# Kernel optimization log

Measured on AMD Instinct MI355X. Metric: run time of the kernel, lower is better.

## Reference

```python
import jax, jax.numpy as jnp
import numpy as np

N_NODES = 100_000
N_EDGES = 1_000_000
H = 128
NUM_STATES = 4
UPPER_T, LOWER_T, NUM_ITERS, TEMP_EVAL = 1.0, 0.1, 10000, 0.1


def temp_by_step(step, upper, lower, num_iters, temp_eval):
    # Python-level schedule: eval temp at step == -1, else linear anneal.
    if step == -1:
        return temp_eval
    frac = min(step / num_iters, 1.0)
    return upper + (lower - upper) * frac


def from_binary_states(states):
    # [*, k] bits -> integer id in [0, 2**k)
    weights = 2 ** jnp.arange(states.shape[-1])
    return (states * weights).sum(-1)


def setup_inputs() -> dict:
    key = jax.random.key(0)
    ks = jax.random.split(key, 20)
    N, E, h = N_NODES, N_EDGES, H
    node_states = jax.random.randint(ks[0], (N, NUM_STATES), 0, 2)
    edge_states = jax.random.randint(ks[1], (E, NUM_STATES), 0, 2)
    scalars = jax.random.normal(ks[2], (E, 1), jnp.float32)
    # first N edges are self-loops ordered by node id (required by the module's
    # node_scalars = scalars[src == dst] indexing convention)
    loops = jnp.arange(N)
    src = jax.random.randint(ks[3], (E - N,), 0, N)
    dst = jax.random.randint(ks[4], (E - N,), 0, N)
    dst = jnp.where(dst == src, (dst + 1) % N, dst)  # no accidental self-loops
    edge_index = jnp.stack([jnp.concatenate([loops, src]),
                            jnp.concatenate([loops, dst])])
    batched_reverse_idx = jax.random.randint(ks[5], (E,), 0, E)
    batch_scalars = jax.random.normal(ks[6], (E, 1, 1), jnp.float32)
    s = 0.02
    params = dict(
        node_emb=s * jax.random.normal(ks[7], (2 ** NUM_STATES, h), jnp.float32),
        edge_emb=s * jax.random.normal(ks[8], (2 ** NUM_STATES, h), jnp.float32),
        combine_W=s * jax.random.normal(ks[9], (2 * h, h), jnp.float32),
        combine_b=jnp.zeros((h,), jnp.float32),
        keep_W=s * jax.random.normal(ks[10], (h, 2), jnp.float32),
        keep_b=jnp.zeros((2,), jnp.float32),
        push_W=s * jax.random.normal(ks[11], (h, 2), jnp.float32),
        push_b=jnp.zeros((2,), jnp.float32),
        push_node_W=s * jax.random.normal(ks[12], (h, 2), jnp.float32),
        push_node_b=jnp.zeros((2,), jnp.float32),
        increment_W=s * jax.random.normal(ks[13], (h, 2), jnp.float32),
        increment_b=jnp.zeros((2,), jnp.float32),
    )
    return dict(node_states=node_states, edge_states=edge_states, scalars=scalars,
                edge_index=edge_index, batched_reverse_idx=batched_reverse_idx,
                batch_scalars=batch_scalars, processor_step=0, training_step=0,
                **params)


def reference(node_states, edge_states, scalars, edge_index, batched_reverse_idx,
              batch_scalars, processor_step, training_step,
              node_emb, edge_emb, combine_W, combine_b, keep_W, keep_b,
              push_W, push_b, push_node_W, push_node_b,
              increment_W, increment_b):
    N = node_states.shape[0]
    tau = temp_by_step(int(training_step), UPPER_T, LOWER_T, NUM_ITERS, TEMP_EVAL)
    # use_noise = config.use_noise (False) and training_step != -1 -> False

    node_fts = node_emb[from_binary_states(node_states)]   # [N, h]
    edge_fts = edge_emb[from_binary_states(edge_states)]   # [E, h]
    src, dst = edge_index[0], edge_index[1]
    fts = jnp.concatenate([edge_fts[batched_reverse_idx], node_fts[src]], axis=1)
    fts = fts @ combine_W + combine_b                       # [E, h]

    s = scalars.reshape(-1)                                 # [E]

    def pair_gumbel_first(W, b):
        # grouped (per-edge pair) softmax; take first component (== [::2])
        logits = (fts @ W + b) / tau                        # [E, 2]
        return jax.nn.softmax(logits, axis=-1)[:, 0]

    increment = 1.0 * pair_gumbel_first(increment_W, increment_b)
    keep = s * pair_gumbel_first(keep_W, keep_b)

    # push: first N edges are self-loops, self-loop of node i is edge i
    push_wo = pair_gumbel_first(push_W, push_b)
    push_w = pair_gumbel_first(push_node_W, push_node_b)
    node_scalars = s[:N]                                    # scalars at self-loops
    s_wo = s - node_scalars[dst]
    s_w = s_wo + node_scalars[src]
    acc = (jax.ops.segment_sum(push_wo * s_wo, dst, num_segments=N)
           + jax.ops.segment_sum(push_w * s_w, dst, num_segments=N))  # [N]
    edge_push = jnp.zeros_like(s).at[:N].set(acc)           # nonzero only on self-loops

    new_scalars = (increment + keep + edge_push)[:, None]   # [E, 1]
    target = batch_scalars[:, processor_step]               # [E, 1]
    loss = jnp.mean((target - new_scalars) ** 2)
    return new_scalars, loss
```

## Files before the change

kernel.cpp:

```cpp
#include <hip/hip_runtime.h>
#include <math.h>
#include <stdint.h>

#define N_NODES 100000
#define N_EDGES 1000000
#define N_NONLOOP (N_EDGES - N_NODES)
#define NXCD 8

#define NP    16
#define PSZ   6250
#define PCAP  61440
#define GOWN  16
#define PROW  6272

#define ACC_SCALE   1048576.0f
#define ACC_INV     (1.0f / 1048576.0f)

typedef float  vfloat4 __attribute__((ext_vector_type(4)));
typedef int    vint4   __attribute__((ext_vector_type(4)));
typedef unsigned long long u64;

#define XCC_ID_HWREG (20 | ((4 - 1) << 11))
__device__ __forceinline__ int get_xcc() {
    return __builtin_amdgcn_s_getreg(XCC_ID_HWREG) & (NXCD - 1);
}
__device__ __forceinline__ void l2_atomic_add_u32(uint32_t* p, uint32_t v) {
    asm volatile("global_atomic_add %0, %1, off" :: "v"(p), "v"(v) : "memory");
}
__device__ __forceinline__ void l2_atomic_add_f32(float* p, float v) {
    asm volatile("global_atomic_add_f32 %0, %1, off" :: "v"(p), "v"(v) : "memory");
}

__device__ __forceinline__ float get_invtau(const int* __restrict__ training_step) {
    int step = training_step[0];
    float tau;
    if (step == -1) {
        tau = 0.1f;
    } else {
        float frac = fminf((float)step / 10000.0f, 1.0f);
        tau = 1.0f + (0.1f - 1.0f) * frac;
    }
    return 1.0f / tau;
}

__device__ __forceinline__ float wave_reduce(float v) {
    #pragma unroll
    for (int off = 32; off > 0; off >>= 1) v += __shfl_down(v, off, 64);
    return v;
}

#define TAB_BLOCKS  132
#define NODE_BLOCKS 391
#define EI_BLOCKS   977

__global__ __launch_bounds__(256) void fused_pre(
    const int* __restrict__ node_states,
    const int* __restrict__ edge_states,
    const float* __restrict__ node_emb,
    const float* __restrict__ edge_emb,
    const float* __restrict__ cW, const float* __restrict__ cb,
    const float* __restrict__ kW, const float* __restrict__ kb,
    const float* __restrict__ pW, const float* __restrict__ pb,
    const float* __restrict__ pnW, const float* __restrict__ pnb,
    const float* __restrict__ iW, const float* __restrict__ ib,
    const int* __restrict__ tstep,
    uint32_t* __restrict__ acc,
    uint32_t* __restrict__ cnt,
    uint8_t* __restrict__ ei,
    uint8_t* __restrict__ nib,
    float* __restrict__ tabs,
    float* __restrict__ lossp,
    float* __restrict__ loss_out,
    int ncopies)
{
    const int b = blockIdx.x;

    if (b < TAB_BLOCKS) {
        const int w    = b;
        const int lane = threadIdx.x & 63;
        const int wv   = threadIdx.x >> 6;
        const float invtau = get_invtau(tstep);
        __shared__ float part[4];

        float p = 0.f;
        if (w < 128) {
            const int isB = w >> 6, h = (w >> 4) & 3, i = w & 15;
            const float* emb = isB ? node_emb : edge_emb;
            const float* cWh = cW + isB * 128 * 128;
            float t0 = 0.f, t1 = 0.f;
            const int l0 = wv * 32;
            #pragma unroll 8
            for (int l = l0; l < l0 + 32; ++l) {
                const float el = emb[i * 128 + l];
                t0 += el * cWh[l * 128 + lane];
                t1 += el * cWh[l * 128 + 64 + lane];
            }
            const float* W = (h == 0) ? kW : (h == 1) ? pW : (h == 2) ? pnW : iW;
            const float wd0 = W[2 * lane] - W[2 * lane + 1];
            const float wd1 = W[2 * (lane + 64)] - W[2 * (lane + 64) + 1];
            p = t0 * wd0 + t1 * wd1;
        } else if (wv == 0) {
            const int h = w & 3;
            const float* W = (h == 0) ? kW : (h == 1) ? pW : (h == 2) ? pnW : iW;
            const float wd0 = W[2 * lane] - W[2 * lane + 1];
            const float wd1 = W[2 * (lane + 64)] - W[2 * (lane + 64) + 1];
            p = cb[lane] * wd0 + cb[64 + lane] * wd1;
        }
        p = wave_reduce(p);
        if (lane == 0) part[wv] = p;
        __syncthreads();
        if (threadIdx.x == 0) {
            const float tot = part[0] + part[1] + part[2] + part[3];
            if (w < 128) {
                const int isB = w >> 6, h = (w >> 4) & 3, i = w & 15;
                tabs[isB * 64 + i * 4 + h] = tot * invtau;
            } else {
                const int h = w & 3;
                const float* bb = (h == 0) ? kb : (h == 1) ? pb : (h == 2) ? pnb : ib;
                tabs[128 + h] = (tot + bb[0] - bb[1]) * invtau;
            }
        }
        return;
    }

    if (b < TAB_BLOCKS + NODE_BLOCKS) {
        const int n = (b - TAB_BLOCKS) * 256 + threadIdx.x;
        if (n < 256) lossp[n] = 0.f;
        if (n == 0) *loss_out = 0.f;
        if (ncopies == 0) {
            if (n < NP) cnt[n] = 0u;
        }
        if (n < N_NODES) {
            vint4 st = __builtin_nontemporal_load(&((const vint4*)node_states)[n]);
            nib[n] = (uint8_t)(st.x + 2 * st.y + 4 * st.z + 8 * st.w);
            for (int k = 0; k < ncopies; ++k) acc[(size_t)k * N_NODES + n] = 0u;
        }
        return;
    }

    const int t = (b - TAB_BLOCKS - NODE_BLOCKS) * 256 + threadIdx.x;
    if (t < N_EDGES / 4) {
        const vint4* esp = (const vint4*)edge_states + 4 * t;
        vint4 e0 = __builtin_nontemporal_load(esp + 0);
        vint4 e1 = __builtin_nontemporal_load(esp + 1);
        vint4 e2 = __builtin_nontemporal_load(esp + 2);
        vint4 e3 = __builtin_nontemporal_load(esp + 3);
        const uint32_t i0 = e0.x + 2 * e0.y + 4 * e0.z + 8 * e0.w;
        const uint32_t i1 = e1.x + 2 * e1.y + 4 * e1.z + 8 * e1.w;
        const uint32_t i2 = e2.x + 2 * e2.y + 4 * e2.z + 8 * e2.w;
        const uint32_t i3 = e3.x + 2 * e3.y + 4 * e3.z + 8 * e3.w;
        ((uint32_t*)ei)[t] = i0 | (i1 << 8) | (i2 << 16) | (i3 << 24);
    }
}

#define EPT 8
__global__ __launch_bounds__(256) void edge_compact(
    const float* __restrict__ s,
    const int* __restrict__ src,
    const int* __restrict__ dst,
    const int* __restrict__ brev,
    const uint8_t* __restrict__ ei,
    const uint8_t* __restrict__ nib,
    const float* __restrict__ tabs,
    const float* __restrict__ target,
    uint32_t* __restrict__ cnt,
    u64* __restrict__ pairs,
    float* __restrict__ lossp,
    float* __restrict__ out)
{
    __shared__ float4 sf[33];
    __shared__ uint32_t lbase[NP], loff[NP];
    const int tid = threadIdx.x;
    if (tid < 33) sf[tid] = ((const float4*)tabs)[tid];
    if (tid < NP) loff[tid] = 0u;
    __syncthreads();

    const int t = blockIdx.x * 256 + tid;
    const bool active = (t < N_NONLOOP / EPT);
    float lsum = 0.f;
    float    ov[EPT], av[EPT];
    int      pj[EPT];
    uint32_t kj[EPT], dloc[EPT];
    int g0 = 0;

    if (active) {
        g0 = (N_NODES / 4) + 2 * t;
        const vint4   rva = __builtin_nontemporal_load(&((const vint4*)brev)[g0]);
        const vint4   rvb = __builtin_nontemporal_load(&((const vint4*)brev)[g0 + 1]);
        const vint4   sra = __builtin_nontemporal_load(&((const vint4*)src)[g0]);
        const vint4   srb = __builtin_nontemporal_load(&((const vint4*)src)[g0 + 1]);
        const vint4   dsa = __builtin_nontemporal_load(&((const vint4*)dst)[g0]);
        const vint4   dsb = __builtin_nontemporal_load(&((const vint4*)dst)[g0 + 1]);
        const vfloat4 sva = __builtin_nontemporal_load(&((const vfloat4*)s)[g0]);
        const vfloat4 svb = __builtin_nontemporal_load(&((const vfloat4*)s)[g0 + 1]);
        const vfloat4 tga = __builtin_nontemporal_load(&((const vfloat4*)target)[g0]);
        const vfloat4 tgb = __builtin_nontemporal_load(&((const vfloat4*)target)[g0 + 1]);

        const int rvv[EPT] = {rva.x, rva.y, rva.z, rva.w, rvb.x, rvb.y, rvb.z, rvb.w};
        const int srv[EPT] = {sra.x, sra.y, sra.z, sra.w, srb.x, srb.y, srb.z, srb.w};
        const int dsv[EPT] = {dsa.x, dsa.y, dsa.z, dsa.w, dsb.x, dsb.y, dsb.z, dsb.w};
        const float svv[EPT] = {sva.x, sva.y, sva.z, sva.w, svb.x, svb.y, svb.z, svb.w};
        const float tgv[EPT] = {tga.x, tga.y, tga.z, tga.w, tgb.x, tgb.y, tgb.z, tgb.w};

        int   eidx[EPT], ni[EPT];
        float ss[EPT], sd[EPT];
        #pragma unroll
        for (int j = 0; j < EPT; ++j) {
            eidx[j] = ei[rvv[j]];
            ni[j]   = nib[srv[j]];
            ss[j]   = s[srv[j]];
            sd[j]   = s[dsv[j]];
        }

        const float4 c4 = sf[32];
        #pragma unroll
        for (int j = 0; j < EPT; ++j) {
            const float4 a = sf[eidx[j]];
            const float4 b = sf[16 + ni[j]];
            const float lk  = a.x + b.x + c4.x;
            const float lp  = a.y + b.y + c4.y;
            const float lpn = a.z + b.z + c4.z;
            const float li  = a.w + b.w + c4.w;
            const float pk  = 1.f / (1.f + __expf(-lk));
            const float pp  = 1.f / (1.f + __expf(-lp));
            const float ppn = 1.f / (1.f + __expf(-lpn));
            const float pi  = 1.f / (1.f + __expf(-li));

            const float s_wo = svv[j] - sd[j];
            const float s_w  = s_wo + ss[j];
            av[j] = pp * s_wo + ppn * s_w;

            const uint32_t p = (uint32_t)dsv[j] / (uint32_t)PSZ;
            pj[j]   = (int)p;
            dloc[j] = (uint32_t)dsv[j] - p * (uint32_t)PSZ;

            ov[j] = pi + svv[j] * pk;
            const float d = tgv[j] - ov[j];
            lsum += d * d;
        }

        #pragma unroll
        for (int j = 0; j < EPT; ++j) kj[j] = atomicAdd(&loff[pj[j]], 1u);
    }

    __syncthreads();
    if (tid < NP) lbase[tid] = atomicAdd(&cnt[tid], loff[tid]);
    __syncthreads();

    if (active) {
        #pragma unroll
        for (int j = 0; j < EPT; ++j) {
            const uint32_t slot = lbase[pj[j]] + kj[j];
            if (slot < PCAP)
                pairs[(size_t)pj[j] * PCAP + slot] =
                    ((u64)dloc[j] << 32) | (uint32_t)__float_as_int(av[j]);
        }
        vfloat4 o4a = {ov[0], ov[1], ov[2], ov[3]};
        vfloat4 o4b = {ov[4], ov[5], ov[6], ov[7]};
        __builtin_nontemporal_store(o4a, &((vfloat4*)out)[g0]);
        __builtin_nontemporal_store(o4b, &((vfloat4*)out)[g0 + 1]);
    }

    lsum = wave_reduce(lsum);
    if ((tid & 63) == 0)
        atomicAdd(&lossp[(blockIdx.x & 15) * 16], lsum);
}

__global__ __launch_bounds__(256) void bin_accum(
    const u64* __restrict__ pairs,
    const uint32_t* __restrict__ cnt,
    float* __restrict__ partials)
{
    __shared__ float part[PROW];
    const int tid = threadIdx.x;
    const int p = blockIdx.x >> 4, r = blockIdx.x & 15;

    for (int k = tid; k < PROW; k += 256) part[k] = 0.f;
    __syncthreads();

    uint32_t c = cnt[p];
    if (c > PCAP) c = PCAP;
    const uint32_t chunk = (c + GOWN - 1) / GOWN;
    const uint32_t lo = r * chunk;
    uint32_t hi = lo + chunk;
    if (hi > c) hi = c;

    const u64* pp = pairs + (size_t)p * PCAP;
    for (uint32_t i = lo + tid; i < hi; i += 256) {
        const u64 v = pp[i];
        atomicAdd(&part[(uint32_t)(v >> 32)], __int_as_float((int)(uint32_t)v));
    }
    __syncthreads();

    float* row = partials + (size_t)blockIdx.x * PROW;
    for (int k = tid; k < PSZ; k += 256) row[k] = part[k];
}

__global__ __launch_bounds__(256) void finalize_binned(
    const float* __restrict__ s,
    const int* __restrict__ brev,
    const uint8_t* __restrict__ ei,
    const uint8_t* __restrict__ nib,
    const float* __restrict__ tabs,
    const float* __restrict__ target,
    const float* __restrict__ partials,
    const float* __restrict__ lossp,
    float* __restrict__ out,
    float* __restrict__ loss_out)
{
    __shared__ float4 sf[33];
    if (threadIdx.x < 33) sf[threadIdx.x] = ((const float4*)tabs)[threadIdx.x];
    __syncthreads();

    const int n = blockIdx.x * blockDim.x + threadIdx.x;
    const bool active = (n < N_NODES);
    float sq = 0.f, v = 0.f;
    if (active) {
        const int  eidx = ei[brev[n]];
        const int  ni   = nib[n];
        const float sv  = s[n];

        const uint32_t p   = (uint32_t)n / (uint32_t)PSZ;
        const uint32_t off = (uint32_t)n - p * PSZ;
        const float* pr = partials + (size_t)p * GOWN * PROW + off;
        float a8 = 0.f;
        #pragma unroll
        for (int r = 0; r < GOWN; ++r) a8 += pr[(size_t)r * PROW];

        const float4 a  = sf[eidx];
        const float4 b  = sf[16 + ni];
        const float4 c4 = sf[32];
        const float lk  = a.x + b.x + c4.x;
        const float lpn = a.z + b.z + c4.z;
        const float li  = a.w + b.w + c4.w;
        const float pk  = 1.f / (1.f + __expf(-lk));
        const float ppn = 1.f / (1.f + __expf(-lpn));
        const float pi  = 1.f / (1.f + __expf(-li));

        v = pi + sv * (pk + ppn) + a8;
        const float d = target[n] - v;
        sq = d * d;
    }
    sq = wave_reduce(sq);
    __shared__ float wsum[4];
    const int lane = threadIdx.x & 63, wid = threadIdx.x >> 6;
    if (lane == 0) wsum[wid] = sq;
    __syncthreads();
    if (threadIdx.x == 0) {
        float tot = (wsum[0] + wsum[1] + wsum[2] + wsum[3]) * (1.0f / (float)N_EDGES);
        if (blockIdx.x == 0) {
            #pragma unroll
            for (int c = 0; c < 16; ++c) tot += lossp[c * 16] * (1.0f / (float)N_EDGES);
        }
        atomicAdd(loss_out, tot);
    }
    if (active) out[n] = v;
}

template<int MODE>
__global__ __launch_bounds__(256) void edge_kernel(
    const float* __restrict__ s,
    const int* __restrict__ src,
    const int* __restrict__ dst,
    const int* __restrict__ brev,
    const uint8_t* __restrict__ ei,
    const uint8_t* __restrict__ nib,
    const float* __restrict__ tabs,
    const float* __restrict__ target,
    uint32_t* __restrict__ acc,
    float* __restrict__ lossp,
    float* __restrict__ out,
    float* __restrict__ loss_out)
{
    __shared__ float4 sf[MODE ? 160 : 33];
    if (threadIdx.x < 33) sf[threadIdx.x] = ((const float4*)tabs)[threadIdx.x];
    __syncthreads();

    int xcc = 0;
    uint32_t* accx = acc;
    if (MODE == 1) {
        xcc  = get_xcc();
        accx = acc + (size_t)xcc * N_NODES;
    }

    const int t = blockIdx.x * blockDim.x + threadIdx.x;
    const bool active = (t < N_NONLOOP / 4);
    float lsum = 0.f;
    float ov[4];
    int   iv[4];
    int   dsv[4];
    int   g = 0;

    if (active) {
        g = (N_NODES / 4) + t;
        const vint4   rv = __builtin_nontemporal_load(&((const vint4*)brev)[g]);
        const vint4   sr = __builtin_nontemporal_load(&((const vint4*)src)[g]);
        const vint4   ds = __builtin_nontemporal_load(&((const vint4*)dst)[g]);
        const vfloat4 sv = __builtin_nontemporal_load(&((const vfloat4*)s)[g]);
        const vfloat4 tg = __builtin_nontemporal_load(&((const vfloat4*)target)[g]);

        const int rvv[4] = {rv.x, rv.y, rv.z, rv.w};
        const int srv[4] = {sr.x, sr.y, sr.z, sr.w};
        dsv[0] = ds.x; dsv[1] = ds.y; dsv[2] = ds.z; dsv[3] = ds.w;
        const float svv[4] = {sv.x, sv.y, sv.z, sv.w};
        const float tgv[4] = {tg.x, tg.y, tg.z, tg.w};

        int   eidx[4], ni[4];
        float ss[4], sd[4];
        #pragma unroll
        for (int j = 0; j < 4; ++j) {
            eidx[j] = ei[rvv[j]];
            ni[j]   = nib[srv[j]];
            ss[j]   = s[srv[j]];
            sd[j]   = s[dsv[j]];
        }

        const float4 c4 = sf[32];
        #pragma unroll
        for (int j = 0; j < 4; ++j) {
            const float4 a = sf[eidx[j]];
            const float4 b = sf[16 + ni[j]];
            const float lk  = a.x + b.x + c4.x;
            const float lp  = a.y + b.y + c4.y;
            const float lpn = a.z + b.z + c4.z;
            const float li  = a.w + b.w + c4.w;
            const float pk  = 1.f / (1.f + __expf(-lk));
            const float pp  = 1.f / (1.f + __expf(-lp));
            const float ppn = 1.f / (1.f + __expf(-lpn));
            const float pi  = 1.f / (1.f + __expf(-li));

            const float s_wo = svv[j] - sd[j];
            const float s_w  = s_wo + ss[j];
            iv[j] = __float2int_rn((pp * s_wo + ppn * s_w) * ACC_SCALE);

            ov[j] = pi + svv[j] * pk;
            const float d = tgv[j] - ov[j];
            lsum += d * d;
        }
    }

    lsum = wave_reduce(lsum);
    __shared__ float wsum[4];
    const int lane = threadIdx.x & 63, wid = threadIdx.x >> 6;
    if (lane == 0) wsum[wid] = lsum;
    __syncthreads();
    if (threadIdx.x == 0) {
        const float tot = (wsum[0] + wsum[1] + wsum[2] + wsum[3]) * (1.0f / (float)N_EDGES);
        if (MODE == 1) l2_atomic_add_f32(&lossp[xcc * 32], tot);
        else           atomicAdd(loss_out, tot);
    }

    if (active) {
        #pragma unroll
        for (int j = 0; j < 4; ++j) {
            if (MODE == 1) l2_atomic_add_u32(&accx[dsv[j]], (uint32_t)iv[j]);
            else           atomicAdd((unsigned int*)&acc[dsv[j]], (unsigned int)iv[j]);
        }
        vfloat4 o4 = {ov[0], ov[1], ov[2], ov[3]};
        __builtin_nontemporal_store(o4, &((vfloat4*)out)[g]);
    }
}

template<int NC>
__global__ __launch_bounds__(256) void finalize_nodes(
    const float* __restrict__ s,
    const int* __restrict__ brev,
    const uint8_t* __restrict__ ei,
    const uint8_t* __restrict__ nib,
    const float* __restrict__ tabs,
    const float* __restrict__ target,
    const uint32_t* __restrict__ acc,
    const float* __restrict__ lossp,
    float* __restrict__ out,
    float* __restrict__ loss_out)
{
    __shared__ float4 sf[33];
    if (threadIdx.x < 33) sf[threadIdx.x] = ((const float4*)tabs)[threadIdx.x];
    __syncthreads();

    const int n = blockIdx.x * blockDim.x + threadIdx.x;
    const bool active = (n < N_NODES);
    float sq = 0.f, v = 0.f;
    if (active) {
        const int  eidx = ei[brev[n]];
        const int  ni   = nib[n];
        const float sv  = s[n];

        uint32_t asum = 0u;
        #pragma unroll
        for (int k = 0; k < NC; ++k) asum += acc[(size_t)k * N_NODES + n];
        const float a8 = (float)(int)asum * ACC_INV;

        const float4 a  = sf[eidx];
        const float4 b  = sf[16 + ni];
        const float4 c4 = sf[32];
        const float lk  = a.x + b.x + c4.x;
        const float lpn = a.z + b.z + c4.z;
        const float li  = a.w + b.w + c4.w;
        const float pk  = 1.f / (1.f + __expf(-lk));
        const float ppn = 1.f / (1.f + __expf(-lpn));
        const float pi  = 1.f / (1.f + __expf(-li));

        v = pi + sv * (pk + ppn) + a8;
        const float d = target[n] - v;
        sq = d * d;
    }
    sq = wave_reduce(sq);
    __shared__ float wsum[4];
    const int lane = threadIdx.x & 63, wid = threadIdx.x >> 6;
    if (lane == 0) wsum[wid] = sq;
    __syncthreads();
    if (threadIdx.x == 0) {
        float tot = (wsum[0] + wsum[1] + wsum[2] + wsum[3]) * (1.0f / (float)N_EDGES);
        if (blockIdx.x == 0) {
            #pragma unroll
            for (int k = 0; k < NXCD; ++k) tot += lossp[k * 32];
        }
        atomicAdd(loss_out, tot);
    }
    if (active) out[n] = v;
}

extern "C" void kernel_launch(void* const* d_in, const int* in_sizes, int n_in,
                              void* d_out, int out_size, void* d_ws, size_t ws_size,
                              hipStream_t stream) {
    const int*   node_states   = (const int*)d_in[0];
    const int*   edge_states   = (const int*)d_in[1];
    const float* scalars       = (const float*)d_in[2];
    const int*   edge_index    = (const int*)d_in[3];
    const int*   brev          = (const int*)d_in[4];
    const float* batch_scalars = (const float*)d_in[5];
    const int*   training_step = (const int*)d_in[7];
    const float* node_emb  = (const float*)d_in[8];
    const float* edge_emb  = (const float*)d_in[9];
    const float* combine_W = (const float*)d_in[10];
    const float* combine_b = (const float*)d_in[11];
    const float* keep_W  = (const float*)d_in[12];
    const float* keep_b  = (const float*)d_in[13];
    const float* push_W  = (const float*)d_in[14];
    const float* push_b  = (const float*)d_in[15];
    const float* pushn_W = (const float*)d_in[16];
    const float* pushn_b = (const float*)d_in[17];
    const float* inc_W   = (const float*)d_in[18];
    const float* inc_b   = (const float*)d_in[19];

    float* out = (float*)d_out;

    const int* srcp = edge_index;
    const int* dstp = edge_index + N_EDGES;

    const size_t PAIRS_B    = (size_t)NP * PCAP * 8;
    const size_t PARTIALS_B = (size_t)NP * GOWN * PROW * 4;
    const size_t need_binned = 3072 + PAIRS_B + PARTIALS_B + N_EDGES + N_NODES;
    const size_t need_scoped = 2048 + (size_t)NXCD * N_NODES * 4 + N_EDGES + N_NODES;

    char* ws = (char*)d_ws;

    if (ws_size >= need_binned) {
        float*    tabs     = (float*)ws;
        float*    lossp    = (float*)(ws + 1024);
        uint32_t* cnt      = (uint32_t*)(ws + 2048);
        u64*      pairs    = (u64*)(ws + 3072);
        float*    partials = (float*)(ws + 3072 + PAIRS_B);
        uint8_t*  ei       = (uint8_t*)(ws + 3072 + PAIRS_B + PARTIALS_B);
        uint8_t*  nib      = ei + N_EDGES;

        fused_pre<<<TAB_BLOCKS + NODE_BLOCKS + EI_BLOCKS, 256, 0, stream>>>(
            node_states, edge_states, node_emb, edge_emb,
            combine_W, combine_b, keep_W, keep_b, push_W, push_b,
            pushn_W, pushn_b, inc_W, inc_b, training_step,
            nullptr, cnt, ei, nib, tabs, lossp, out + N_EDGES, 0);

        const int ethreads8 = N_NONLOOP / EPT;
        edge_compact<<<(ethreads8 + 255) / 256, 256, 0, stream>>>(
            scalars, srcp, dstp, brev, ei, nib, tabs, batch_scalars,
            cnt, pairs, lossp, out);

        bin_accum<<<NP * GOWN, 256, 0, stream>>>(pairs, cnt, partials);

        finalize_binned<<<(N_NODES + 255) / 256, 256, 0, stream>>>(
            scalars, brev, ei, nib, tabs, batch_scalars, partials, lossp,
            out, out + N_EDGES);
    } else {
        const bool scoped = (ws_size >= need_scoped);
        const int nc = scoped ? NXCD : 1;

        float*    tabs  = (float*)ws;
        float*    lossp = (float*)(ws + 1024);
        uint32_t* acc   = (uint32_t*)(ws + 2048);
        uint8_t*  ei    = (uint8_t*)(ws + 2048 + (size_t)nc * N_NODES * 4);
        uint8_t*  nib   = ei + N_EDGES;

        fused_pre<<<TAB_BLOCKS + NODE_BLOCKS + EI_BLOCKS, 256, 0, stream>>>(
            node_states, edge_states, node_emb, edge_emb,
            combine_W, combine_b, keep_W, keep_b, push_W, push_b,
            pushn_W, pushn_b, inc_W, inc_b, training_step,
            acc, nullptr, ei, nib, tabs, lossp, out + N_EDGES, nc);

        const int ethreads = N_NONLOOP / 4;
        const int eblocks  = (ethreads + 255) / 256;
        if (scoped) {
            edge_kernel<1><<<eblocks, 256, 0, stream>>>(
                scalars, srcp, dstp, brev, ei, nib, tabs, batch_scalars,
                acc, lossp, out, out + N_EDGES);
            finalize_nodes<NXCD><<<(N_NODES + 255) / 256, 256, 0, stream>>>(
                scalars, brev, ei, nib, tabs, batch_scalars, acc, lossp,
                out, out + N_EDGES);
        } else {
            edge_kernel<0><<<eblocks, 256, 0, stream>>>(
                scalars, srcp, dstp, brev, ei, nib, tabs, batch_scalars,
                acc, lossp, out, out + N_EDGES);
            finalize_nodes<1><<<(N_NODES + 255) / 256, 256, 0, stream>>>(
                scalars, brev, ei, nib, tabs, batch_scalars, acc, lossp,
                out, out + N_EDGES);
        }
    }
}
```

Before: 156.7 us.

## Fuse bin accumulation and node finalize via per-partition completion counters

Merges the bin_accum and finalize_binned kernels into a single bin_fin kernel, dropping one launch. The 16 blocks of each partition signal completion through an agent-scope atomic counter and spin until all 16 have written their partial rows. Each block then sums the partials and finalizes its 391-node slice. This removes a kernel launch and its boundary, but depends on all 256 blocks being resident at once to avoid deadlock, and adds spin-wait and memory-fence cost.

Result: slower. 163.5 us (+4.3%).

```diff
diff --git a/kernel.cpp b/kernel.cpp
--- a/kernel.cpp
+++ b/kernel.cpp
@@ -12,6 +12,7 @@
 #define PCAP  61440
 #define GOWN  16
 #define PROW  6272
+#define NCHUNK 391
 
 #define ACC_SCALE   1048576.0f
 #define ACC_INV     (1.0f / 1048576.0f)
@@ -66,6 +67,7 @@
     const int* __restrict__ tstep,
     uint32_t* __restrict__ acc,
     uint32_t* __restrict__ cnt,
+    uint32_t* __restrict__ done,
     uint8_t* __restrict__ ei,
     uint8_t* __restrict__ nib,
     float* __restrict__ tabs,
@@ -129,6 +131,7 @@
         if (n == 0) *loss_out = 0.f;
         if (ncopies == 0) {
             if (n < NP) cnt[n] = 0u;
+            if (n >= 32 && n < 32 + NP) done[n - 32] = 0u;
         }
         if (n < N_NODES) {
             vint4 st = __builtin_nontemporal_load(&((const vint4*)node_states)[n]);
@@ -266,15 +269,27 @@
         atomicAdd(&lossp[(blockIdx.x & 15) * 16], lsum);
 }
 
-__global__ __launch_bounds__(256) void bin_accum(
+__global__ __launch_bounds__(256) void bin_fin(
     const u64* __restrict__ pairs,
     const uint32_t* __restrict__ cnt,
-    float* __restrict__ partials)
+    uint32_t* __restrict__ done,
+    float* __restrict__ partials,
+    const float* __restrict__ s,
+    const int* __restrict__ brev,
+    const uint8_t* __restrict__ ei,
+    const uint8_t* __restrict__ nib,
+    const float* __restrict__ tabs,
+    const float* __restrict__ target,
+    const float* __restrict__ lossp,
+    float* __restrict__ out,
+    float* __restrict__ loss_out)
 {
     __shared__ float part[PROW];
+    __shared__ float4 sf[33];
     const int tid = threadIdx.x;
     const int p = blockIdx.x >> 4, r = blockIdx.x & 15;
 
+    if (tid < 33) sf[tid] = ((const float4*)tabs)[tid];
     for (int k = tid; k < PROW; k += 256) part[k] = 0.f;
     __syncthreads();
 
@@ -294,38 +309,31 @@
 
     float* row = partials + (size_t)blockIdx.x * PROW;
     for (int k = tid; k < PSZ; k += 256) row[k] = part[k];
-}
-
-__global__ __launch_bounds__(256) void finalize_binned(
-    const float* __restrict__ s,
-    const int* __restrict__ brev,
-    const uint8_t* __restrict__ ei,
-    const uint8_t* __restrict__ nib,
-    const float* __restrict__ tabs,
-    const float* __restrict__ target,
-    const float* __restrict__ partials,
-    const float* __restrict__ lossp,
-    float* __restrict__ out,
-    float* __restrict__ loss_out)
-{
-    __shared__ float4 sf[33];
-    if (threadIdx.x < 33) sf[threadIdx.x] = ((const float4*)tabs)[threadIdx.x];
-    __syncthreads();
-
-    const int n = blockIdx.x * blockDim.x + threadIdx.x;
-    const bool active = (n < N_NODES);
-    float sq = 0.f, v = 0.f;
-    if (active) {
+
+    __syncthreads();
+    if (tid == 0) {
+        __hip_atomic_fetch_add(&done[p], 1u, __ATOMIC_RELEASE,
+                               __HIP_MEMORY_SCOPE_AGENT);
+        while (__hip_atomic_load(&done[p], __ATOMIC_ACQUIRE,
+                                 __HIP_MEMORY_SCOPE_AGENT) < GOWN)
+            __builtin_amdgcn_s_sleep(8);
+    }
+    __syncthreads();
+
+    const int klo = r * NCHUNK;
+    const int khi = (klo + NCHUNK < PSZ) ? klo + NCHUNK : PSZ;
+    const float* prp = partials + (size_t)p * GOWN * PROW;
+    float sq = 0.f;
+
+    for (int k = klo + tid; k < khi; k += 256) {
+        const int n = p * PSZ + k;
         const int  eidx = ei[brev[n]];
         const int  ni   = nib[n];
         const float sv  = s[n];
 
-        const uint32_t p   = (uint32_t)n / (uint32_t)PSZ;
-        const uint32_t off = (uint32_t)n - p * PSZ;
-        const float* pr = partials + (size_t)p * GOWN * PROW + off;
-        float a8 = 0.f;
-        #pragma unroll
-        for (int r = 0; r < GOWN; ++r) a8 += pr[(size_t)r * PROW];
+        float a16 = 0.f;
+        #pragma unroll
+        for (int rr = 0; rr < GOWN; ++rr) a16 += prp[(size_t)rr * PROW + k];
 
         const float4 a  = sf[eidx];
         const float4 b  = sf[16 + ni];
@@ -337,24 +345,26 @@
         const float ppn = 1.f / (1.f + __expf(-lpn));
         const float pi  = 1.f / (1.f + __expf(-li));
 
-        v = pi + sv * (pk + ppn) + a8;
+        const float v = pi + sv * (pk + ppn) + a16;
+        out[n] = v;
         const float d = target[n] - v;
-        sq = d * d;
-    }
+        sq += d * d;
+    }
+
     sq = wave_reduce(sq);
     __shared__ float wsum[4];
-    const int lane = threadIdx.x & 63, wid = threadIdx.x >> 6;
+    const int lane = tid & 63, wid = tid >> 6;
     if (lane == 0) wsum[wid] = sq;
     __syncthreads();
-    if (threadIdx.x == 0) {
+    if (tid == 0) {
         float tot = (wsum[0] + wsum[1] + wsum[2] + wsum[3]) * (1.0f / (float)N_EDGES);
         if (blockIdx.x == 0) {
             #pragma unroll
-            for (int c = 0; c < 16; ++c) tot += lossp[c * 16] * (1.0f / (float)N_EDGES);
+            for (int cix = 0; cix < 16; ++cix)
+                tot += lossp[cix * 16] * (1.0f / (float)N_EDGES);
         }
         atomicAdd(loss_out, tot);
     }
-    if (active) out[n] = v;
 }
 
 template<int MODE>
@@ -560,6 +570,7 @@
         float*    tabs     = (float*)ws;
         float*    lossp    = (float*)(ws + 1024);
         uint32_t* cnt      = (uint32_t*)(ws + 2048);
+        uint32_t* done     = (uint32_t*)(ws + 2048 + 512);
         u64*      pairs    = (u64*)(ws + 3072);
         float*    partials = (float*)(ws + 3072 + PAIRS_B);
         uint8_t*  ei       = (uint8_t*)(ws + 3072 + PAIRS_B + PARTIALS_B);
@@ -569,18 +580,16 @@
             node_states, edge_states, node_emb, edge_emb,
             combine_W, combine_b, keep_W, keep_b, push_W, push_b,
             pushn_W, pushn_b, inc_W, inc_b, training_step,
-            nullptr, cnt, ei, nib, tabs, lossp, out + N_EDGES, 0);
+            nullptr, cnt, done, ei, nib, tabs, lossp, out + N_EDGES, 0);
 
         const int ethreads8 = N_NONLOOP / EPT;
         edge_compact<<<(ethreads8 + 255) / 256, 256, 0, stream>>>(
             scalars, srcp, dstp, brev, ei, nib, tabs, batch_scalars,
             cnt, pairs, lossp, out);
 
-        bin_accum<<<NP * GOWN, 256, 0, stream>>>(pairs, cnt, partials);
-
-        finalize_binned<<<(N_NODES + 255) / 256, 256, 0, stream>>>(
-            scalars, brev, ei, nib, tabs, batch_scalars, partials, lossp,
-            out, out + N_EDGES);
+        bin_fin<<<NP * GOWN, 256, 0, stream>>>(
+            pairs, cnt, done, partials, scalars, brev, ei, nib, tabs,
+            batch_scalars, lossp, out, out + N_EDGES);
     } else {
         const bool scoped = (ws_size >= need_scoped);
         const int nc = scoped ? NXCD : 1;
@@ -595,7 +604,7 @@
             node_states, edge_states, node_emb, edge_emb,
             combine_W, combine_b, keep_W, keep_b, push_W, push_b,
             pushn_W, pushn_b, inc_W, inc_b, training_step,
-            acc, nullptr, ei, nib, tabs, lossp, out + N_EDGES, nc);
+            acc, nullptr, nullptr, ei, nib, tabs, lossp, out + N_EDGES, nc);
 
         const int ethreads = N_NONLOOP / 4;
         const int eblocks  = (ethreads + 255) / 256;
```
